# Optimization experiments

Hardware: AMD Instinct MI355X
Metric: run time of the kernel (lower is better)

The kernel has to match this reference:

```python
import jax, jax.numpy as jnp
import numpy as np

B, N, IN, HID, H, OUT = 32, 512, 64, 64, 4, 64
NEG_SLOPE = 0.2
NEG_INF = -1e9


def setup_inputs() -> dict:
    key = jax.random.key(0)
    ks = jax.random.split(key, 10)
    s = 0.1
    return {
        "x": jax.random.normal(ks[0], (B, N, IN), jnp.float32),
        "adj": jax.random.randint(ks[1], (B, N, N), 0, 2, jnp.int32),
        "W1": jax.random.normal(ks[2], (IN, H * HID), jnp.float32) * s,
        "a1_src": jax.random.normal(ks[3], (H, HID), jnp.float32) * s,
        "a1_dst": jax.random.normal(ks[4], (H, HID), jnp.float32) * s,
        "b1": jnp.zeros((H * HID,), jnp.float32),
        "W2": jax.random.normal(ks[5], (H * HID, OUT), jnp.float32) * s,
        "a2_src": jax.random.normal(ks[6], (1, OUT), jnp.float32) * s,
        "a2_dst": jax.random.normal(ks[7], (1, OUT), jnp.float32) * s,
        "b2": jnp.zeros((OUT,), jnp.float32),
    }


def _gat_layer(x, mask, W, a_src, a_dst, b, heads, feat):
    # x: [N, Fin]; mask: [N_dst, N_src] bool (edge src->dst), self-loops included
    h = (x @ W).reshape(N, heads, feat)              # [N, H, F]
    e_src = jnp.einsum('nhf,hf->nh', h, a_src)       # [N, H]
    e_dst = jnp.einsum('nhf,hf->nh', h, a_dst)       # [N, H]
    # scores[d, s, h] = leaky_relu(a_dst.x_d + a_src.x_s)
    scores = jax.nn.leaky_relu(e_dst[:, None, :] + e_src[None, :, :], NEG_SLOPE)
    scores = jnp.where(mask[:, :, None], scores, NEG_INF)
    alpha = jax.nn.softmax(scores, axis=1)           # segment-softmax over src neighbors
    out = jnp.einsum('dsh,shf->dhf', alpha, h)       # aggregate messages
    return out.reshape(N, heads * feat) + b


def reference(x, adj, W1, a1_src, a1_dst, b1, W2, a2_src, a2_dst, b2):
    eye = jnp.eye(N, dtype=bool)

    def one_graph(xi, ai):
        # edge i->j when adj[i, j] != 0 (coo row=src, col=dst); add self-loops
        mask = (ai != 0).T | eye                     # [dst, src]
        h1 = jax.nn.elu(_gat_layer(xi, mask, W1, a1_src, a1_dst, b1, H, HID))
        return _gat_layer(h1, mask, W2, a2_src, a2_dst, b2, 1, OUT)

    return jax.vmap(one_graph)(x, adj)               # [B, N, OUT]
```

## Files before the change

### kernel.cpp

```cpp
#include <hip/hip_runtime.h>
#include <cstddef>

#define NN 512
#define NEG_SLOPE 0.2f

typedef __attribute__((ext_vector_type(8))) short short8;
typedef __attribute__((ext_vector_type(16))) float f32x16;

__device__ __forceinline__ unsigned short f2bf(float v) {
  unsigned u = __float_as_uint(v);
  return (unsigned short)((u + 0x7FFFu + ((u >> 16) & 1u)) >> 16);
}

__global__ __launch_bounds__(256) void k_prep(
    const int* __restrict__ adj, const float* __restrict__ W1,
    const float* __restrict__ a1s, const float* __restrict__ a1d,
    const float* __restrict__ W2, const float* __restrict__ a2s,
    const float* __restrict__ a2d, unsigned* __restrict__ mask,
    short8* __restrict__ W1B, short8* __restrict__ W2B) {
  int blk = blockIdx.x, t = threadIdx.x;
  if (blk < 512) {
    int b = blk >> 4, w = blk & 15;
    const int* base = adj + (size_t)b * NN * NN + (size_t)w * 32 * NN;
#pragma unroll
    for (int half = 0; half < 2; ++half) {
      int d = t + half * 256;
      unsigned wv = 0;
#pragma unroll
      for (int j = 0; j < 32; ++j) {
        unsigned bit = ((base[(size_t)j * NN + d] != 0) || (w * 32 + j == d)) ? 1u : 0u;
        wv |= bit << j;
      }
      mask[((size_t)b * 16 + w) * NN + d] = wv;
    }
  } else if (blk < 521) {
    int blk2 = blk - 512;
    if (blk2 < 8) {
      int idx = blk2 * 256 + t;
      int unit = idx >> 6, lane = idx & 63;
      int nt = unit >> 2, kt = unit & 3;
      int f = nt * 32 + (lane & 31);
      int k0 = kt * 16 + ((lane >> 5) << 3);
      short8 r;
#pragma unroll
      for (int j = 0; j < 8; ++j) r[j] = (short)f2bf(W1[(k0 + j) * 256 + f]);
      W1B[idx] = r;
    } else {
      __shared__ float wa1[64][8];
#pragma unroll
      for (int rep = 0; rep < 2; ++rep) {
        int id = t + rep * 256;
        int k = id >> 3, c = id & 7, h = c & 3;
        const float* av = ((c < 4) ? a1s : a1d) + h * 64;
        float s = 0.f;
        for (int f2 = 0; f2 < 64; ++f2) s += W1[k * 256 + h * 64 + f2] * av[f2];
        wa1[k][c] = s;
      }
      __syncthreads();
      int kt = t >> 6, lane = t & 63, col = lane & 31, kg = lane >> 5;
      short8 r;
#pragma unroll
      for (int j = 0; j < 8; ++j)
        r[j] = (col < 8) ? (short)f2bf(wa1[kt * 16 + kg * 8 + j][col]) : (short)0;
      W1B[2048 + t] = r;
    }
  } else {
    int blk3 = blk - 521;
    if (blk3 < 8) {
      int idx = blk3 * 256 + t;
      int unit = idx >> 6, lane = idx & 63;
      int nt = unit >> 4, kt = unit & 15;
      int f = nt * 32 + (lane & 31);
      int k0 = kt * 16 + ((lane >> 5) << 3);
      short8 r;
#pragma unroll
      for (int j = 0; j < 8; ++j) r[j] = (short)f2bf(W2[(k0 + j) * 64 + f]);
      W2B[idx] = r;
    } else {
      __shared__ float wa2[64][2];
      int kbase = (blk3 - 8) * 64;
      if (t < 128) {
        int k = t >> 1, c = t & 1;
        const float* av = (c == 0) ? a2s : a2d;
        float s = 0.f;
        for (int f2 = 0; f2 < 64; ++f2) s += W2[(kbase + k) * 64 + f2] * av[f2];
        wa2[k][c] = s;
      }
      __syncthreads();
      int ktl = t >> 6, lane = t & 63, col = lane & 31, kg = lane >> 5;
      short8 r;
#pragma unroll
      for (int j = 0; j < 8; ++j)
        r[j] = (col < 2) ? (short)f2bf(wa2[ktl * 16 + kg * 8 + j][col]) : (short)0;
      W2B[2048 + (blk3 - 8) * 256 + t] = r;
    }
  }
}

__global__ __launch_bounds__(64) void k_gemm1(const float* __restrict__ x,
                                              const short8* __restrict__ W1B,
                                              unsigned short* __restrict__ hb1,
                                              float* __restrict__ e1s,
                                              float* __restrict__ e1d) {
  __shared__ float tile[32 * 33];
  int i = blockIdx.x;
  int b = (i & 7) * 4 + ((i >> 3) & 3), mt = i >> 5;
  int lane = threadIdx.x, m = lane & 31, kg = lane >> 5;
  const float* xrow = x + ((size_t)b * NN + mt * 32 + m) * 64 + kg * 8;
  short8 a[4];
#pragma unroll
  for (int kt = 0; kt < 4; ++kt) {
    float4 v0 = *(const float4*)(xrow + kt * 16);
    float4 v1 = *(const float4*)(xrow + kt * 16 + 4);
    short8 r;
    r[0] = (short)f2bf(v0.x); r[1] = (short)f2bf(v0.y);
    r[2] = (short)f2bf(v0.z); r[3] = (short)f2bf(v0.w);
    r[4] = (short)f2bf(v1.x); r[5] = (short)f2bf(v1.y);
    r[6] = (short)f2bf(v1.z); r[7] = (short)f2bf(v1.w);
    a[kt] = r;
  }
  short8* hb8 = (short8*)hb1;
  for (int nt = 0; nt < 9; ++nt) {
    f32x16 acc;
#pragma unroll
    for (int q = 0; q < 16; ++q) acc[q] = 0.f;
#pragma unroll
    for (int kt = 0; kt < 4; ++kt)
      acc = __builtin_amdgcn_mfma_f32_32x32x16_bf16(
          a[kt], W1B[(nt * 4 + kt) * 64 + lane], acc, 0, 0, 0);
    if (nt < 8) {
#pragma unroll
      for (int reg = 0; reg < 16; ++reg) {
        int row = (reg & 3) + 8 * (reg >> 2) + 4 * kg;
        tile[row * 33 + m] = acc[reg];
      }
      __syncthreads();
      int h = nt >> 1, ft = nt & 1;
#pragma unroll
      for (int ktl = 0; ktl < 2; ++ktl) {
        short8 r;
#pragma unroll
        for (int j = 0; j < 8; ++j)
          r[j] = (short)f2bf(tile[(ktl * 16 + kg * 8 + j) * 33 + m]);
        hb8[((((size_t)b * 4 + h) * 32 + mt * 2 + ktl) * 2 + ft) * 64 + lane] = r;
      }
      __syncthreads();
    } else {
      if (m < 8) {
        float* p = ((m < 4) ? e1s : e1d) + ((size_t)b * 4 + (m & 3)) * NN + mt * 32;
#pragma unroll
        for (int reg = 0; reg < 16; ++reg) {
          int row = (reg & 3) + 8 * (reg >> 2) + 4 * kg;
          p[row] = acc[reg];
        }
      }
    }
  }
}

__global__ __launch_bounds__(256) void k_attn1g2(const unsigned* __restrict__ mask,
                                                 const unsigned short* __restrict__ hb1,
                                                 const float* __restrict__ e1s,
                                                 const float* __restrict__ e1d,
                                                 const float* __restrict__ b1,
                                                 const short8* __restrict__ W2B,
                                                 unsigned short* __restrict__ hb2,
                                                 float* __restrict__ e2s,
                                                 float* __restrict__ e2d) {
  __shared__ float es[4 * NN];
  __shared__ unsigned mw[16 * 32];
  __shared__ unsigned short ht[32 * 264];
  __shared__ float tile2[2 * 32 * 33];
  int i = blockIdx.x;
  int b = (i & 7) * 4 + ((i >> 3) & 3), mt = i >> 5;
  int d0 = mt * 32;
  int t = threadIdx.x;
  const float* esrc = e1s + (size_t)b * 4 * NN;
#pragma unroll
  for (int q = 0; q < 8; ++q) es[t + q * 256] = esrc[t + q * 256];
  const unsigned* msrc = mask + (size_t)b * 16 * NN + d0;
  mw[t] = msrc[(t >> 5) * NN + (t & 31)];
  {
    int idx = t + 256;
    mw[idx] = msrc[(idx >> 5) * NN + (idx & 31)];
  }
  __syncthreads();
  int h = t >> 6, lane = t & 63, m = lane & 31, kg = lane >> 5;
  float ed = e1d[((size_t)b * 4 + h) * NN + d0 + m];
  const short8* bfr = (const short8*)hb1 + ((size_t)b * 4 + h) * 32 * 2 * 64;
  f32x16 acc0, acc1;
#pragma unroll
  for (int q = 0; q < 16; ++q) { acc0[q] = 0.f; acc1[q] = 0.f; }
  float l = 0.f;
  for (int kt = 0; kt < 32; ++kt) {
    unsigned wv = mw[(kt >> 1) * 32 + m];
    int shift = (kt & 1) * 16 + kg * 8;
    const float* ep = &es[h * NN + kt * 16 + kg * 8];
    short8 a;
#pragma unroll
    for (int j = 0; j < 8; ++j) {
      float sc = ed + ep[j];
      sc = fmaxf(sc, NEG_SLOPE * sc);
      float pv = __expf(sc);
      pv = ((wv >> (shift + j)) & 1u) ? pv : 0.f;
      l += pv;
      a[j] = (short)f2bf(pv);
    }
    short8 bv0 = bfr[(kt * 2 + 0) * 64 + lane];
    short8 bv1 = bfr[(kt * 2 + 1) * 64 + lane];
    acc0 = __builtin_amdgcn_mfma_f32_32x32x16_bf16(a, bv0, acc0, 0, 0, 0);
    acc1 = __builtin_amdgcn_mfma_f32_32x32x16_bf16(a, bv1, acc1, 0, 0, 0);
  }
  float lf = l + __shfl(l, lane ^ 32, 64);
  float linv = 1.f / lf;
  float bia0 = b1[h * 64 + m];
  float bia1 = b1[h * 64 + 32 + m];
#pragma unroll
  for (int reg = 0; reg < 16; ++reg) {
    int row = (reg & 3) + 8 * (reg >> 2) + 4 * kg;
    float li = __shfl(linv, row, 64);
    float v0 = acc0[reg] * li + bia0;
    v0 = (v0 > 0.f) ? v0 : (__expf(v0) - 1.f);
    float v1 = acc1[reg] * li + bia1;
    v1 = (v1 > 0.f) ? v1 : (__expf(v1) - 1.f);
    ht[row * 264 + h * 64 + m] = f2bf(v0);
    ht[row * 264 + h * 64 + 32 + m] = f2bf(v1);
  }
  __syncthreads();
  int w2 = t >> 6, lane2 = t & 63, m2 = lane2 & 31, kg2 = lane2 >> 5;
  if (w2 < 3) {
    int nt = w2;
    f32x16 acc;
#pragma unroll
    for (int q = 0; q < 16; ++q) acc[q] = 0.f;
#pragma unroll
    for (int kt = 0; kt < 16; ++kt) {
      short8 av = *(const short8*)&ht[m2 * 264 + kt * 16 + kg2 * 8];
      acc = __builtin_amdgcn_mfma_f32_32x32x16_bf16(
          av, W2B[(nt * 16 + kt) * 64 + lane2], acc, 0, 0, 0);
    }
    if (nt < 2) {
      float* tw = tile2 + nt * (32 * 33);
#pragma unroll
      for (int reg = 0; reg < 16; ++reg) {
        int row = (reg & 3) + 8 * (reg >> 2) + 4 * kg2;
        tw[row * 33 + m2] = acc[reg];
      }
      short8* hb8 = (short8*)hb2;
#pragma unroll
      for (int ktl = 0; ktl < 2; ++ktl) {
        short8 r;
#pragma unroll
        for (int j = 0; j < 8; ++j)
          r[j] = (short)f2bf(tw[(ktl * 16 + kg2 * 8 + j) * 33 + m2]);
        hb8[(((size_t)b * 32 + mt * 2 + ktl) * 2 + nt) * 64 + lane2] = r;
      }
    } else {
      if (m2 < 2) {
        float* p = ((m2 == 0) ? e2s : e2d) + (size_t)b * NN + mt * 32;
#pragma unroll
        for (int reg = 0; reg < 16; ++reg) {
          int row = (reg & 3) + 8 * (reg >> 2) + 4 * kg2;
          p[row] = acc[reg];
        }
      }
    }
  }
}

__global__ __launch_bounds__(256) void k_attn2(const unsigned* __restrict__ mask,
                                               const unsigned short* __restrict__ hb2,
                                               const float* __restrict__ e2s,
                                               const float* __restrict__ e2d,
                                               const float* __restrict__ b2,
                                               float* __restrict__ out) {
  __shared__ float es[NN];
  __shared__ unsigned mw[16 * 32];
  __shared__ float cred[4][2][16][64];
  __shared__ float lred[4][64];
  __shared__ float linv_s[32];
  int i = blockIdx.x;
  int b = (i & 7) * 4 + ((i >> 3) & 3);
  int d0 = (i >> 5) * 32;
  int t = threadIdx.x;
  es[t] = e2s[(size_t)b * NN + t];
  es[t + 256] = e2s[(size_t)b * NN + t + 256];
  const unsigned* msrc = mask + (size_t)b * 16 * NN + d0;
  mw[t] = msrc[(t >> 5) * NN + (t & 31)];
  {
    int idx = t + 256;
    mw[idx] = msrc[(idx >> 5) * NN + (idx & 31)];
  }
  __syncthreads();
  int w = t >> 6, lane = t & 63, m = lane & 31, kg = lane >> 5;
  float ed = e2d[(size_t)b * NN + d0 + m];
  const short8* bfr = (const short8*)hb2 + (size_t)b * 32 * 2 * 64;
  f32x16 acc0, acc1;
#pragma unroll
  for (int q = 0; q < 16; ++q) { acc0[q] = 0.f; acc1[q] = 0.f; }
  float l = 0.f;
#pragma unroll
  for (int kk = 0; kk < 8; ++kk) {
    int kt = w * 8 + kk;
    unsigned wv = mw[(kt >> 1) * 32 + m];
    int shift = (kt & 1) * 16 + kg * 8;
    const float* ep = &es[kt * 16 + kg * 8];
    short8 a;
#pragma unroll
    for (int j = 0; j < 8; ++j) {
      float sc = ed + ep[j];
      sc = fmaxf(sc, NEG_SLOPE * sc);
      float pv = __expf(sc);
      pv = ((wv >> (shift + j)) & 1u) ? pv : 0.f;
      l += pv;
      a[j] = (short)f2bf(pv);
    }
    short8 bv0 = bfr[(kt * 2 + 0) * 64 + lane];
    short8 bv1 = bfr[(kt * 2 + 1) * 64 + lane];
    acc0 = __builtin_amdgcn_mfma_f32_32x32x16_bf16(a, bv0, acc0, 0, 0, 0);
    acc1 = __builtin_amdgcn_mfma_f32_32x32x16_bf16(a, bv1, acc1, 0, 0, 0);
  }
  lred[w][lane] = l;
#pragma unroll
  for (int reg = 0; reg < 16; ++reg) {
    cred[w][0][reg][lane] = acc0[reg];
    cred[w][1][reg][lane] = acc1[reg];
  }
  __syncthreads();
  if (t < 32) {
    float s = 0.f;
#pragma unroll
    for (int q = 0; q < 4; ++q) s += lred[q][t] + lred[q][t + 32];
    linv_s[t] = 1.f / s;
  }
  __syncthreads();
#pragma unroll
  for (int q = 0; q < 8; ++q) {
    int pos = t + q * 256;
    int nt = pos >> 10;
    int rem = pos & 1023;
    int reg = rem >> 6;
    int ln = rem & 63;
    float v = cred[0][nt][reg][ln] + cred[1][nt][reg][ln] +
              cred[2][nt][reg][ln] + cred[3][nt][reg][ln];
    int row = (reg & 3) + 8 * (reg >> 2) + 4 * (ln >> 5);
    int col = nt * 32 + (ln & 31);
    out[((size_t)b * NN + d0 + row) * 64 + col] = v * linv_s[row] + b2[col];
  }
}

extern "C" void kernel_launch(void* const* d_in, const int* in_sizes, int n_in,
                              void* d_out, int out_size, void* d_ws, size_t ws_size,
                              hipStream_t stream) {
  const float* x = (const float*)d_in[0];
  const int* adj = (const int*)d_in[1];
  const float* W1 = (const float*)d_in[2];
  const float* a1s = (const float*)d_in[3];
  const float* a1d = (const float*)d_in[4];
  const float* b1 = (const float*)d_in[5];
  const float* W2 = (const float*)d_in[6];
  const float* a2s = (const float*)d_in[7];
  const float* a2d = (const float*)d_in[8];
  const float* b2 = (const float*)d_in[9];
  float* out = (float*)d_out;

  char* w = (char*)d_ws;
  unsigned* mask = (unsigned*)w;
  short8* W1B = (short8*)(w + (3u << 20));
  short8* W2B = (short8*)(w + (3u << 20) + (64u << 10));
  unsigned short* hb1 = (unsigned short*)(w + (4u << 20));
  float* e1s = (float*)(w + (12u << 20));
  float* e1d = (float*)(w + (12u << 20) + (256u << 10));
  unsigned short* hb2 = (unsigned short*)(w + (21u << 20));
  float* e2s = (float*)(w + (23u << 20));
  float* e2d = (float*)(w + (23u << 20) + (64u << 10));

  hipLaunchKernelGGL(k_prep, dim3(533), dim3(256), 0, stream, adj, W1, a1s,
                     a1d, W2, a2s, a2d, mask, W1B, W2B);
  hipLaunchKernelGGL(k_gemm1, dim3(512), dim3(64), 0, stream, x, W1B, hb1,
                     e1s, e1d);
  hipLaunchKernelGGL(k_attn1g2, dim3(512), dim3(256), 0, stream, mask, hb1,
                     e1s, e1d, b1, W2B, hb2, e2s, e2d);
  hipLaunchKernelGGL(k_attn2, dim3(512), dim3(256), 0, stream, mask, hb2, e2s,
                     e2d, b2, out);
}
```

Measured before the change: 133.3 us.

## Fuse mask packing and weight conversion into GEMM1 kernel, drop prep launch

Removes the separate prep kernel. Adjacency mask packing now runs in three spare waves of the layer-1 GEMM kernel, and W1/W2 are converted to bf16 fragments inline from fp32 global memory. Attention source and destination scores are now computed from the fp32 projected tile with a dot against a_src/a_dst, instead of an extra MFMA against precomputed W·a columns. This saves one launch and the extra MFMA N-tile, but each block redoes the weight conversion, and the single GEMM wave per block may now wait on the mask work in the same block.

```diff
diff --git a/kernel.cpp b/kernel.cpp
--- a/kernel.cpp
+++ b/kernel.cpp
@@ -12,101 +12,40 @@
   return (unsigned short)((u + 0x7FFFu + ((u >> 16) & 1u)) >> 16);
 }
 
-__global__ __launch_bounds__(256) void k_prep(
-    const int* __restrict__ adj, const float* __restrict__ W1,
-    const float* __restrict__ a1s, const float* __restrict__ a1d,
-    const float* __restrict__ W2, const float* __restrict__ a2s,
-    const float* __restrict__ a2d, unsigned* __restrict__ mask,
-    short8* __restrict__ W1B, short8* __restrict__ W2B) {
-  int blk = blockIdx.x, t = threadIdx.x;
-  if (blk < 512) {
-    int b = blk >> 4, w = blk & 15;
-    const int* base = adj + (size_t)b * NN * NN + (size_t)w * 32 * NN;
-#pragma unroll
-    for (int half = 0; half < 2; ++half) {
-      int d = t + half * 256;
+__global__ __launch_bounds__(256) void k_g1m(const int* __restrict__ adj,
+                                             const float* __restrict__ x,
+                                             const float* __restrict__ W1,
+                                             const float* __restrict__ a1s,
+                                             const float* __restrict__ a1d,
+                                             unsigned* __restrict__ mask,
+                                             unsigned short* __restrict__ hb1,
+                                             float* __restrict__ e1s,
+                                             float* __restrict__ e1d) {
+  __shared__ float tile[32 * 36];
+  int i = blockIdx.x;
+  int b = (i & 7) * 4 + ((i >> 3) & 3), mt = i >> 5;
+  int d0 = mt * 32;
+  int t = threadIdx.x;
+
+  if (t >= 64) {
+    int t2 = t - 64;
+    const int* abase = adj + (size_t)b * NN * NN;
+    for (int u = t2; u < 512; u += 192) {
+      int d = d0 + (u & 31), w = u >> 5;
       unsigned wv = 0;
 #pragma unroll
       for (int j = 0; j < 32; ++j) {
-        unsigned bit = ((base[(size_t)j * NN + d] != 0) || (w * 32 + j == d)) ? 1u : 0u;
+        int s = w * 32 + j;
+        unsigned bit = ((abase[(size_t)s * NN + d] != 0) || (s == d)) ? 1u : 0u;
         wv |= bit << j;
       }
       mask[((size_t)b * 16 + w) * NN + d] = wv;
     }
-  } else if (blk < 521) {
-    int blk2 = blk - 512;
-    if (blk2 < 8) {
-      int idx = blk2 * 256 + t;
-      int unit = idx >> 6, lane = idx & 63;
-      int nt = unit >> 2, kt = unit & 3;
-      int f = nt * 32 + (lane & 31);
-      int k0 = kt * 16 + ((lane >> 5) << 3);
-      short8 r;
-#pragma unroll
-      for (int j = 0; j < 8; ++j) r[j] = (short)f2bf(W1[(k0 + j) * 256 + f]);
-      W1B[idx] = r;
-    } else {
-      __shared__ float wa1[64][8];
-#pragma unroll
-      for (int rep = 0; rep < 2; ++rep) {
-        int id = t + rep * 256;
-        int k = id >> 3, c = id & 7, h = c & 3;
-        const float* av = ((c < 4) ? a1s : a1d) + h * 64;
-        float s = 0.f;
-        for (int f2 = 0; f2 < 64; ++f2) s += W1[k * 256 + h * 64 + f2] * av[f2];
-        wa1[k][c] = s;
-      }
-      __syncthreads();
-      int kt = t >> 6, lane = t & 63, col = lane & 31, kg = lane >> 5;
-      short8 r;
-#pragma unroll
-      for (int j = 0; j < 8; ++j)
-        r[j] = (col < 8) ? (short)f2bf(wa1[kt * 16 + kg * 8 + j][col]) : (short)0;
-      W1B[2048 + t] = r;
-    }
-  } else {
-    int blk3 = blk - 521;
-    if (blk3 < 8) {
-      int idx = blk3 * 256 + t;
-      int unit = idx >> 6, lane = idx & 63;
-      int nt = unit >> 4, kt = unit & 15;
-      int f = nt * 32 + (lane & 31);
-      int k0 = kt * 16 + ((lane >> 5) << 3);
-      short8 r;
-#pragma unroll
-      for (int j = 0; j < 8; ++j) r[j] = (short)f2bf(W2[(k0 + j) * 64 + f]);
-      W2B[idx] = r;
-    } else {
-      __shared__ float wa2[64][2];
-      int kbase = (blk3 - 8) * 64;
-      if (t < 128) {
-        int k = t >> 1, c = t & 1;
-        const float* av = (c == 0) ? a2s : a2d;
-        float s = 0.f;
-        for (int f2 = 0; f2 < 64; ++f2) s += W2[(kbase + k) * 64 + f2] * av[f2];
-        wa2[k][c] = s;
-      }
-      __syncthreads();
-      int ktl = t >> 6, lane = t & 63, col = lane & 31, kg = lane >> 5;
-      short8 r;
-#pragma unroll
-      for (int j = 0; j < 8; ++j)
-        r[j] = (col < 2) ? (short)f2bf(wa2[ktl * 16 + kg * 8 + j][col]) : (short)0;
-      W2B[2048 + (blk3 - 8) * 256 + t] = r;
-    }
-  }
-}
-
-__global__ __launch_bounds__(64) void k_gemm1(const float* __restrict__ x,
-                                              const short8* __restrict__ W1B,
-                                              unsigned short* __restrict__ hb1,
-                                              float* __restrict__ e1s,
-                                              float* __restrict__ e1d) {
-  __shared__ float tile[32 * 33];
-  int i = blockIdx.x;
-  int b = (i & 7) * 4 + ((i >> 3) & 3), mt = i >> 5;
-  int lane = threadIdx.x, m = lane & 31, kg = lane >> 5;
-  const float* xrow = x + ((size_t)b * NN + mt * 32 + m) * 64 + kg * 8;
+    return;
+  }
+
+  int lane = t, m = lane & 31, kg = lane >> 5;
+  const float* xrow = x + ((size_t)b * NN + d0 + m) * 64 + kg * 8;
   short8 a[4];
 #pragma unroll
   for (int kt = 0; kt < 4; ++kt) {
@@ -120,40 +59,63 @@
     a[kt] = r;
   }
   short8* hb8 = (short8*)hb1;
-  for (int nt = 0; nt < 9; ++nt) {
+  short8 wf[2][4];
+#pragma unroll
+  for (int kt = 0; kt < 4; ++kt) {
+    int k0 = kt * 16 + kg * 8;
+    short8 r;
+#pragma unroll
+    for (int j = 0; j < 8; ++j) r[j] = (short)f2bf(W1[(k0 + j) * 256 + m]);
+    wf[0][kt] = r;
+  }
+  float e_h = 0.f;
+#pragma unroll
+  for (int nt = 0; nt < 8; ++nt) {
+    int cur = nt & 1;
+    if (nt < 7) {
+      int f = (nt + 1) * 32 + m;
+#pragma unroll
+      for (int kt = 0; kt < 4; ++kt) {
+        int k0 = kt * 16 + kg * 8;
+        short8 r;
+#pragma unroll
+        for (int j = 0; j < 8; ++j) r[j] = (short)f2bf(W1[(k0 + j) * 256 + f]);
+        wf[cur ^ 1][kt] = r;
+      }
+    }
     f32x16 acc;
 #pragma unroll
     for (int q = 0; q < 16; ++q) acc[q] = 0.f;
 #pragma unroll
     for (int kt = 0; kt < 4; ++kt)
-      acc = __builtin_amdgcn_mfma_f32_32x32x16_bf16(
-          a[kt], W1B[(nt * 4 + kt) * 64 + lane], acc, 0, 0, 0);
-    if (nt < 8) {
-#pragma unroll
-      for (int reg = 0; reg < 16; ++reg) {
-        int row = (reg & 3) + 8 * (reg >> 2) + 4 * kg;
-        tile[row * 33 + m] = acc[reg];
-      }
-      __syncthreads();
-      int h = nt >> 1, ft = nt & 1;
-#pragma unroll
-      for (int ktl = 0; ktl < 2; ++ktl) {
-        short8 r;
-#pragma unroll
-        for (int j = 0; j < 8; ++j)
-          r[j] = (short)f2bf(tile[(ktl * 16 + kg * 8 + j) * 33 + m]);
-        hb8[((((size_t)b * 4 + h) * 32 + mt * 2 + ktl) * 2 + ft) * 64 + lane] = r;
-      }
-      __syncthreads();
-    } else {
-      if (m < 8) {
-        float* p = ((m < 4) ? e1s : e1d) + ((size_t)b * 4 + (m & 3)) * NN + mt * 32;
-#pragma unroll
-        for (int reg = 0; reg < 16; ++reg) {
-          int row = (reg & 3) + 8 * (reg >> 2) + 4 * kg;
-          p[row] = acc[reg];
-        }
-      }
+      acc = __builtin_amdgcn_mfma_f32_32x32x16_bf16(a[kt], wf[cur][kt], acc, 0, 0, 0);
+#pragma unroll
+    for (int reg = 0; reg < 16; ++reg) {
+      int row = (reg & 3) + 8 * (reg >> 2) + 4 * kg;
+      tile[row * 36 + m] = acc[reg];
+    }
+    int h = nt >> 1, ft = nt & 1;
+#pragma unroll
+    for (int ktl = 0; ktl < 2; ++ktl) {
+      short8 r;
+#pragma unroll
+      for (int j = 0; j < 8; ++j)
+        r[j] = (short)f2bf(tile[(ktl * 16 + kg * 8 + j) * 36 + m]);
+      hb8[((((size_t)b * 4 + h) * 32 + mt * 2 + ktl) * 2 + ft) * 64 + lane] = r;
+    }
+    const float* coeff = (kg ? a1d : a1s) + h * 64 + ft * 32;
+    float ep = 0.f;
+#pragma unroll
+    for (int c4 = 0; c4 < 8; ++c4) {
+      float4 tv = *(const float4*)&tile[m * 36 + c4 * 4];
+      float4 cv = *(const float4*)&coeff[c4 * 4];
+      ep += tv.x * cv.x + tv.y * cv.y + tv.z * cv.z + tv.w * cv.w;
+    }
+    e_h += ep;
+    if (ft) {
+      float* p = kg ? e1d : e1s;
+      p[((size_t)b * 4 + h) * NN + d0 + m] = e_h;
+      e_h = 0.f;
     }
   }
 }
@@ -163,14 +125,16 @@
                                                  const float* __restrict__ e1s,
                                                  const float* __restrict__ e1d,
                                                  const float* __restrict__ b1,
-                                                 const short8* __restrict__ W2B,
+                                                 const float* __restrict__ W2,
+                                                 const float* __restrict__ a2s,
+                                                 const float* __restrict__ a2d,
                                                  unsigned short* __restrict__ hb2,
                                                  float* __restrict__ e2s,
                                                  float* __restrict__ e2d) {
   __shared__ float es[4 * NN];
   __shared__ unsigned mw[16 * 32];
   __shared__ unsigned short ht[32 * 264];
-  __shared__ float tile2[2 * 32 * 33];
+  __shared__ float tile2[2][32 * 36];
   int i = blockIdx.x;
   int b = (i & 7) * 4 + ((i >> 3) & 3), mt = i >> 5;
   int d0 = mt * 32;
@@ -227,43 +191,60 @@
     ht[row * 264 + h * 64 + 32 + m] = f2bf(v1);
   }
   __syncthreads();
-  int w2 = t >> 6, lane2 = t & 63, m2 = lane2 & 31, kg2 = lane2 >> 5;
-  if (w2 < 3) {
+  int w2 = t >> 6;
+  if (w2 < 2) {
     int nt = w2;
+    short8 wfr[16];
+#pragma unroll
+    for (int kt = 0; kt < 16; ++kt) {
+      int k0 = kt * 16 + kg * 8;
+      short8 r;
+#pragma unroll
+      for (int j = 0; j < 8; ++j)
+        r[j] = (short)f2bf(W2[(k0 + j) * 64 + nt * 32 + m]);
+      wfr[kt] = r;
+    }
     f32x16 acc;
 #pragma unroll
     for (int q = 0; q < 16; ++q) acc[q] = 0.f;
 #pragma unroll
     for (int kt = 0; kt < 16; ++kt) {
-      short8 av = *(const short8*)&ht[m2 * 264 + kt * 16 + kg2 * 8];
-      acc = __builtin_amdgcn_mfma_f32_32x32x16_bf16(
-          av, W2B[(nt * 16 + kt) * 64 + lane2], acc, 0, 0, 0);
-    }
-    if (nt < 2) {
-      float* tw = tile2 + nt * (32 * 33);
-#pragma unroll
-      for (int reg = 0; reg < 16; ++reg) {
-        int row = (reg & 3) + 8 * (reg >> 2) + 4 * kg2;
-        tw[row * 33 + m2] = acc[reg];
-      }
-      short8* hb8 = (short8*)hb2;
-#pragma unroll
-      for (int ktl = 0; ktl < 2; ++ktl) {
-        short8 r;
-#pragma unroll
-        for (int j = 0; j < 8; ++j)
-          r[j] = (short)f2bf(tw[(ktl * 16 + kg2 * 8 + j) * 33 + m2]);
-        hb8[(((size_t)b * 32 + mt * 2 + ktl) * 2 + nt) * 64 + lane2] = r;
-      }
-    } else {
-      if (m2 < 2) {
-        float* p = ((m2 == 0) ? e2s : e2d) + (size_t)b * NN + mt * 32;
-#pragma unroll
-        for (int reg = 0; reg < 16; ++reg) {
-          int row = (reg & 3) + 8 * (reg >> 2) + 4 * kg2;
-          p[row] = acc[reg];
-        }
-      }
+      short8 av = *(const short8*)&ht[m * 264 + kt * 16 + kg * 8];
+      acc = __builtin_amdgcn_mfma_f32_32x32x16_bf16(av, wfr[kt], acc, 0, 0, 0);
+    }
+    float* tw = tile2[nt];
+#pragma unroll
+    for (int reg = 0; reg < 16; ++reg) {
+      int row = (reg & 3) + 8 * (reg >> 2) + 4 * kg;
+      tw[row * 36 + m] = acc[reg];
+    }
+  }
+  __syncthreads();
+  if (w2 < 2) {
+    const float* tw = tile2[w2];
+    short8* hb8 = (short8*)hb2;
+#pragma unroll
+    for (int ktl = 0; ktl < 2; ++ktl) {
+      short8 r;
+#pragma unroll
+      for (int j = 0; j < 8; ++j)
+        r[j] = (short)f2bf(tw[(ktl * 16 + kg * 8 + j) * 36 + m]);
+      hb8[(((size_t)b * 32 + mt * 2 + ktl) * 2 + w2) * 64 + lane] = r;
+    }
+  } else {
+    const float* coeff = ((w2 == 2) ? a2s : a2d) + kg * 32;
+    const float* tsrc = tile2[kg];
+    float val = 0.f;
+#pragma unroll
+    for (int c4 = 0; c4 < 8; ++c4) {
+      float4 tv = *(const float4*)&tsrc[m * 36 + c4 * 4];
+      float4 cv = *(const float4*)&coeff[c4 * 4];
+      val += tv.x * cv.x + tv.y * cv.y + tv.z * cv.z + tv.w * cv.w;
+    }
+    float tot = val + __shfl(val, lane ^ 32, 64);
+    if (kg == 0) {
+      float* p = (w2 == 2) ? e2s : e2d;
+      p[(size_t)b * NN + d0 + m] = tot;
     }
   }
 }
@@ -366,8 +347,6 @@
 
   char* w = (char*)d_ws;
   unsigned* mask = (unsigned*)w;
-  short8* W1B = (short8*)(w + (3u << 20));
-  short8* W2B = (short8*)(w + (3u << 20) + (64u << 10));
   unsigned short* hb1 = (unsigned short*)(w + (4u << 20));
   float* e1s = (float*)(w + (12u << 20));
   float* e1d = (float*)(w + (12u << 20) + (256u << 10));
@@ -375,12 +354,10 @@
   float* e2s = (float*)(w + (23u << 20));
   float* e2d = (float*)(w + (23u << 20) + (64u << 10));
 
-  hipLaunchKernelGGL(k_prep, dim3(533), dim3(256), 0, stream, adj, W1, a1s,
-                     a1d, W2, a2s, a2d, mask, W1B, W2B);
-  hipLaunchKernelGGL(k_gemm1, dim3(512), dim3(64), 0, stream, x, W1B, hb1,
-                     e1s, e1d);
+  hipLaunchKernelGGL(k_g1m, dim3(512), dim3(256), 0, stream, adj, x, W1, a1s,
+                     a1d, mask, hb1, e1s, e1d);
   hipLaunchKernelGGL(k_attn1g2, dim3(512), dim3(256), 0, stream, mask, hb1,
-                     e1s, e1d, b1, W2B, hb2, e2s, e2d);
+                     e1s, e1d, b1, W2, a2s, a2d, hb2, e2s, e2d);
   hipLaunchKernelGGL(k_attn2, dim3(512), dim3(256), 0, stream, mask, hb2, e2s,
                      e2d, b2, out);
 }
```

Result: slower. 140.3 us (+5.3%).
